# Kernel tuning notes

Measured on AMD Instinct MI355X. Metric: run time of the kernel, lower is better.

Reference implementation:

```python
import jax, jax.numpy as jnp
import numpy as np

B, H, W, D, C, K, ITERS = 16, 64, 64, 64, 16, 5, 4
EPS_LN = 1e-5

def _ln(x, g, b):
    m = x.mean(-1, keepdims=True)
    v = jnp.mean((x - m) ** 2, axis=-1, keepdims=True)
    return (x - m) / jnp.sqrt(v + EPS_LN) * g + b

def _build_grid(h, w):
    # (h, w, 2) with x in [-1,1] over width, y in [-1,1] over height
    y, x = jnp.meshgrid(jnp.linspace(-1.0, 1.0, h), jnp.linspace(-1.0, 1.0, w), indexing='ij')
    return jnp.stack([x, y], axis=-1)

def _forward(feat, feat_color, mask, slot_noise, slots_mu, slots_logsigma,
             w_grid, b_grid, w_k, w_v, ln_kv_g, ln_kv_b, w_mlp, b_mlp,
             ln_q_g, ln_q_b, w_q, w_ih, w_hh, b_ih, b_hh,
             ln_feat_g, ln_feat_b, ln_color_g, ln_color_b,
             ln_res_g, ln_res_b, w_res, b_res):
    b, h, w, d = feat.shape
    n = h * w
    k_slots = mask.shape[0]
    scale = d ** (-0.5)

    grid = _build_grid(h, w)  # (H, W, 2)

    # fg position: weighted mean of grid under mask -> (K, 2), broadcast to (B, K, 2)
    gm = grid.transpose(2, 0, 1)[None] * mask            # (K, 2, H, W)
    fg_pos = gm.sum((2, 3)) / (mask.sum((2, 3)) + 1e-5)  # (K, 2)
    fg_pos = jnp.broadcast_to(fg_pos[None], (b, k_slots, 2))

    feat_n = _ln(feat.reshape(b, n, d), ln_feat_g, ln_feat_b)                    # (B, N, D)
    featc_n = _ln(feat_color.reshape(b, n, feat_color.shape[-1]), ln_color_g, ln_color_b)

    slot = slots_mu + jnp.exp(slots_logsigma) * slot_noise  # (B, K, D)

    # k/v with relative positional grid embedding (fg_pos is constant across iters,
    # so k/v are iteration-invariant and computed once -- same math as the original loop)
    rel = grid[None, None] - fg_pos[:, :, None, None, :]        # (B, K, H, W, 2)
    rel4 = jnp.concatenate([rel, -rel], -1).reshape(b, k_slots, n, 4)
    grid_embed = rel4 @ w_grid.T + b_grid                       # (B, K, N, D)
    k = _ln(feat_n @ w_k.T[None] [0][None][0][None][0] if False else (feat_n @ w_k.T)[:, None] + grid_embed, ln_kv_g, ln_kv_b) @ w_mlp.T + b_mlp
    v = _ln((feat_n @ w_v.T)[:, None] + grid_embed, ln_kv_g, ln_kv_b) @ w_mlp.T + b_mlp

    attn = None
    for it in range(ITERS):
        prev = slot
        q = _ln(slot, ln_q_g, ln_q_b) @ w_q.T                         # (B, K, D)
        logits = jnp.einsum('bkd,bknd->bkn', q, k) * scale
        attn = jax.nn.softmax(logits, axis=-1)                        # (B, K, N)
        upd = jnp.einsum('bkn,bknd->bkd', attn, v)                    # (B, K, D)
        if it != ITERS - 1:
            # torch GRUCell
            x = upd.reshape(-1, d)
            hp = slot.reshape(-1, d)
            gi = x @ w_ih.T + b_ih
            gh = hp @ w_hh.T + b_hh
            i_r, i_z, i_n = jnp.split(gi, 3, axis=-1)
            h_r, h_z, h_n = jnp.split(gh, 3, axis=-1)
            r = jax.nn.sigmoid(i_r + h_r)
            z = jax.nn.sigmoid(i_z + h_z)
            nn_ = jnp.tanh(i_n + r * h_n)
            slot = ((1.0 - z) * nn_ + z * hp).reshape(b, k_slots, d)
            slot = _ln(slot, ln_res_g, ln_res_b) @ w_res.T + b_res + prev
        else:
            slot_color = jnp.einsum('bkn,bnc->bkc', attn, featc_n)
            slot = jnp.concatenate([slot, slot_color], axis=-1)       # (B, K, D+C)

    amin = attn.min(axis=2, keepdims=True)
    amax = attn.max(axis=2, keepdims=True)
    attn = (attn - amin) / (amax - amin + 1e-5)
    return slot, fg_pos, attn

def setup_inputs() -> dict:
    key = jax.random.key(0)
    ks = jax.random.split(key, 16)
    def rn(i, shape, s=0.02):
        return jax.random.normal(ks[i], shape, jnp.float32) * s
    return {
        'feat': jax.random.normal(ks[0], (B, H, W, D), jnp.float32),
        'feat_color': jax.random.normal(ks[1], (B, H, W, C), jnp.float32),
        'mask': jax.random.uniform(ks[2], (K, 1, H, W), jnp.float32),
        'slot_noise': jax.random.normal(ks[3], (B, K, D), jnp.float32),
        'slots_mu': rn(4, (1, 1, D), 1.0),
        'slots_logsigma': rn(5, (1, 1, D), 0.01),
        'w_grid': rn(6, (D, 4)), 'b_grid': jnp.zeros((D,), jnp.float32),
        'w_k': rn(7, (D, D)), 'w_v': rn(8, (D, D)),
        'ln_kv_g': jnp.ones((D,), jnp.float32), 'ln_kv_b': jnp.zeros((D,), jnp.float32),
        'w_mlp': rn(9, (D, D)), 'b_mlp': jnp.zeros((D,), jnp.float32),
        'ln_q_g': jnp.ones((D,), jnp.float32), 'ln_q_b': jnp.zeros((D,), jnp.float32),
        'w_q': rn(10, (D, D)),
        'w_ih': rn(11, (3 * D, D)), 'w_hh': rn(12, (3 * D, D)),
        'b_ih': jnp.zeros((3 * D,), jnp.float32), 'b_hh': jnp.zeros((3 * D,), jnp.float32),
        'ln_feat_g': jnp.ones((D,), jnp.float32), 'ln_feat_b': jnp.zeros((D,), jnp.float32),
        'ln_color_g': jnp.ones((C,), jnp.float32), 'ln_color_b': jnp.zeros((C,), jnp.float32),
        'ln_res_g': jnp.ones((D,), jnp.float32), 'ln_res_b': jnp.zeros((D,), jnp.float32),
        'w_res': rn(13, (D, D)), 'b_res': jnp.zeros((D,), jnp.float32),
    }

def reference(feat, feat_color, mask, slot_noise, slots_mu, slots_logsigma,
              w_grid, b_grid, w_k, w_v, ln_kv_g, ln_kv_b, w_mlp, b_mlp,
              ln_q_g, ln_q_b, w_q, w_ih, w_hh, b_ih, b_hh,
              ln_feat_g, ln_feat_b, ln_color_g, ln_color_b,
              ln_res_g, ln_res_b, w_res, b_res):
    return _forward(feat, feat_color, mask, slot_noise, slots_mu, slots_logsigma,
                    w_grid, b_grid, w_k, w_v, ln_kv_g, ln_kv_b, w_mlp, b_mlp,
                    ln_q_g, ln_q_b, w_q, w_ih, w_hh, b_ih, b_hh,
                    ln_feat_g, ln_feat_b, ln_color_g, ln_color_b,
                    ln_res_g, ln_res_b, w_res, b_res)
```

## Files before the change

### kernel.cpp

```cpp
#include <hip/hip_runtime.h>
#include <stdint.h>

#define B_ 16
#define H_ 64
#define W_ 64
#define D_ 64
#define C_ 16
#define K_ 5
#define N_ 4096
#define NC_ 32
#define CS_ 128
#define EPS 1e-5f

typedef __attribute__((ext_vector_type(8))) short bf16x8;
typedef __attribute__((ext_vector_type(4))) float f32x4;

__device__ __forceinline__ float wsum64(float v){
  #pragma unroll
  for(int o=1;o<64;o<<=1) v += __shfl_xor(v,o,64);
  return v;
}
__device__ __forceinline__ float wmax64(float v){
  #pragma unroll
  for(int o=1;o<64;o<<=1) v = fmaxf(v, __shfl_xor(v,o,64));
  return v;
}
__device__ __forceinline__ float wmin64(float v){
  #pragma unroll
  for(int o=1;o<64;o<<=1) v = fminf(v, __shfl_xor(v,o,64));
  return v;
}
__device__ __forceinline__ uint16_t f2bf(float f){
  uint32_t u = __float_as_uint(f);
  u += 0x7fffu + ((u>>16)&1u);
  return (uint16_t)(u>>16);
}

__global__ __launch_bounds__(256) void k_pre(
    const float* __restrict__ mask, const float* __restrict__ noise,
    const float* __restrict__ mu, const float* __restrict__ lsg,
    const float* __restrict__ wm, const float* __restrict__ bm, const float* __restrict__ lnkb,
    const float* __restrict__ wk, const float* __restrict__ wv, const float* __restrict__ lnfb,
    const float* __restrict__ wq, const float* __restrict__ lnqg, const float* __restrict__ lnqb,
    const float* __restrict__ wres, const float* __restrict__ bres,
    const float* __restrict__ lnrg, const float* __restrict__ lnrb,
    const float* __restrict__ wih, const float* __restrict__ whh,
    const float* __restrict__ wg, const float* __restrict__ bg,
    float* __restrict__ ws_fg, float* __restrict__ out_fg,
    float* __restrict__ bm2, float* __restrict__ fkb, float* __restrict__ fvb,
    float* __restrict__ qb, float* __restrict__ br2,
    float* __restrict__ wgx, float* __restrict__ wgy, float* __restrict__ gscal,
    float* __restrict__ wqpT, float* __restrict__ wrpT,
    float* __restrict__ wvT, float* __restrict__ wmT,
    float* __restrict__ gw, float* __restrict__ slot, float* __restrict__ out_slot){
  int bid=blockIdx.x, tid=threadIdx.x;
  if(bid<5){
    int k=bid;
    float sm=0.f, sx=0.f, sy=0.f;
    for(int p=tid; p<H_*W_; p+=256){
      int i=p>>6, j=p&63;
      float m = mask[k*H_*W_ + p];
      float x = -1.f + (2.f/63.f)*j;
      float y = -1.f + (2.f/63.f)*i;
      sm+=m; sx+=m*x; sy+=m*y;
    }
    __shared__ float r0[4], r1[4], r2[4];
    int wid=tid>>6, lane=tid&63;
    sm=wsum64(sm); sx=wsum64(sx); sy=wsum64(sy);
    if(lane==0){ r0[wid]=sm; r1[wid]=sx; r2[wid]=sy; }
    __syncthreads();
    if(tid==0){
      float tm=r0[0]+r0[1]+r0[2]+r0[3];
      float tx=r1[0]+r1[1]+r1[2]+r1[3];
      float ty=r2[0]+r2[1]+r2[2]+r2[3];
      float px = tx/(tm+1e-5f), py = ty/(tm+1e-5f);
      ws_fg[k*2+0]=px; ws_fg[k*2+1]=py;
      for(int b=0;b<B_;b++){ out_fg[(b*K_+k)*2+0]=px; out_fg[(b*K_+k)*2+1]=py; }
// ... 18 lines not shown
      t=wsum64(wy);    if(l==0) gscal[1]=t*(1.f/64.f);
      t=wsum64(bl);    if(l==0) gscal[2]=t*(1.f/64.f);
      t=wsum64(wx*wx); if(l==0) gscal[3]=t*(1.f/64.f);
      t=wsum64(wy*wy); if(l==0) gscal[4]=t*(1.f/64.f);
      t=wsum64(wx*wy); if(l==0) gscal[5]=t*(2.f/64.f);
      t=wsum64(wx*bl); if(l==0) gscal[6]=t*(2.f/64.f);
      t=wsum64(wy*bl); if(l==0) gscal[7]=t*(2.f/64.f);
      t=wsum64(bl*bl); if(l==0) gscal[8]=t*(1.f/64.f);
    } else {
      for(int j=l;j<B_*K_*16;j+=64){ int bk2=j>>4, cc2=j&15; out_slot[bk2*80+64+cc2]=0.f; }
    }
  } else if(bid<71){
    int i=(bid-7)*256+tid;
    int a=i>>12, r=i&4095, d=r>>6, o=r&63;
    if(a==0)      wqpT[r]=0.125f*lnqg[d]*wq[o*64+d];
    else if(a==1) wrpT[r]=lnrg[d]*wres[o*64+d];
    else if(a==2) wvT[r]=wv[o*64+d];
    else          wmT[r]=wm[o*64+d];
  } else if(bid<167){
    int i=(bid-71)*256+tid;
    int g6=i>>12, r=i&4095, d=r>>6, o=r&63;
    float v = (g6<3)? wih[(g6*64+o)*64+d] : whh[((g6-3)*64+o)*64+d];
    gw[g6*4096 + d*64 + o] = v;
  } else {
    int i=(bid-167)*256+tid;
    if(i<B_*K_*D_){ int d=i&63; slot[i]=mu[d]+expf(lsg[d])*noise[i]; }
  }
}

__global__ __launch_bounds__(256) void k_featln(const float* __restrict__ feat,
    const float* __restrict__ wk, const float* __restrict__ wv, const float* __restrict__ gf,
    const float* __restrict__ fkb, const float* __restrict__ fvb,
    const float* __restrict__ wgx, const float* __restrict__ wgy, const float* __restrict__ bg,
    const float* __restrict__ fc, const float* __restrict__ gc, const float* __restrict__ bc,
    uint16_t* __restrict__ Aout, float4* __restrict__ kstat, float4* __restrict__ vstat,
    float* __restrict__ fcn){
  int tid=threadIdx.x, wid=tid>>6, lane=tid&63;
  int q=lane>>4, c=lane&15;
  size_t row = (size_t)blockIdx.x*64 + wid*16 + c;
  const float* xp = feat + row*64;
  float x[16];
  *(float4*)&x[0]  = *(const float4*)(xp + q*8);
  *(float4*)&x[4]  = *(const float4*)(xp + q*8 + 4);
  *(float4*)&x[8]  = *(const float4*)(xp + 32 + q*8);
  *(float4*)&x[12] = *(const float4*)(xp + 36 + q*8);
  float s=0.f;
  #pragma unroll
  for(int i=0;i<16;i++) s+=x[i];
  s += __shfl_xor(s,16,64); s += __shfl_xor(s,32,64);
// ... 55 lines not shown
    if(lane<16){
      size_t row2 = (size_t)blockIdx.x*64 + wid*16 + lane;
      float4 st = { ss*(1.f/64.f), s2*(1.f/64.f)+db*(1.f/32.f), dx*(1.f/32.f), dy*(1.f/32.f) };
      (mat? vstat : kstat)[row2] = st;
    }
  }
  int r16=tid>>4, cc=tid&15;
  #pragma unroll
  for(int i=0;i<4;i++){
    size_t row2 = (size_t)blockIdx.x*64 + i*16 + r16;
    float xv = fc[row2*16+cc];
    float sc=xv;
    #pragma unroll
    for(int o=1;o<16;o<<=1) sc += __shfl_xor(sc,o,16);
    float m2 = sc*(1.f/16.f);
    float df = xv-m2;
    float v2 = df*df;
    #pragma unroll
    for(int o=1;o<16;o<<=1) v2 += __shfl_xor(v2,o,16);
    fcn[row2*16+cc] = df*rsqrtf(v2*(1.f/16.f)+EPS)*gc[cc] + bc[cc];
  }
}

template<bool GRU>
__global__ __launch_bounds__(256) void k_slotq(
    const float* __restrict__ slot_prev, float* __restrict__ slot_cur,
    const float* __restrict__ part, const float* __restrict__ pscal,
    const float* __restrict__ red_in,
    const float* __restrict__ gw,
    const float* __restrict__ bih, const float* __restrict__ bhh,
    const float* __restrict__ wrpT, const float* __restrict__ br2,
    const float* __restrict__ wqpT, const float* __restrict__ qb,
    const float* __restrict__ wm, const float* __restrict__ wk,
    const float* __restrict__ lnfg, const float* __restrict__ lnkg,
    const float* __restrict__ fkb, const float* __restrict__ bm2, const float* __restrict__ fvb,
    const float* __restrict__ wvT, const float* __restrict__ wmT,
    const float* __restrict__ wgx, const float* __restrict__ wgy, const float* __restrict__ bg,
    const float* __restrict__ gscal,
    float* __restrict__ qs_out, float* __restrict__ cst_out){
  __shared__ float vv[64], vh[64];
  __shared__ float red6[4][64][6];
  __shared__ float lamb[NC_];
  int bk=blockIdx.x;
  int tid=threadIdx.x, wid=tid>>6, lane=tid&63;
  int o=lane, qq=wid;
  float mwgx=gscal[0], mwgy=gscal[1], mbg=gscal[2];

  #define MV(Wptr) { float p_=0.f; \
      _Pragma("unroll") \
      for(int dd=0;dd<16;dd++) p_ = fmaf(vv[qq*16+dd], (Wptr)[(qq*16+dd)*64+o], p_); \
      red6[qq][o][0]=p_; } __syncthreads();
  #define SUM0 (red6[0][lane][0]+red6[1][lane][0]+red6[2][lane][0]+red6[3][lane][0])

  float cur=0.f, qv=0.f, qp=0.f, hp=0.f;
  if(GRU){
    float As=0.f, Ax=0.f, Ay=0.f, Am=0.f;
    if(wid==0){
      float m_l = (lane<NC_)? red_in[((size_t)bk*NC_+lane)*4]   : -1e30f;
      float s_l = (lane<NC_)? red_in[((size_t)bk*NC_+lane)*4+1] : 0.f;
      float M = wmax64(m_l);
      float eu = (lane<NC_)? __expf(m_l-M) : 0.f;
      float S = wsum64(s_l*eu);
      float lam = eu/S;
      if(lane<NC_) lamb[lane]=lam;
      float p0 = (lane<NC_)? pscal[((size_t)bk*NC_+lane)*4+0] : 0.f;
      float p1 = (lane<NC_)? pscal[((size_t)bk*NC_+lane)*4+1] : 0.f;
      float p2 = (lane<NC_)? pscal[((size_t)bk*NC_+lane)*4+2] : 0.f;
      float p3 = (lane<NC_)? pscal[((size_t)bk*NC_+lane)*4+3] : 0.f;
      As = wsum64(lam*p0); Ax = wsum64(lam*p1);
      Ay = wsum64(lam*p2); Am = wsum64(lam*p3);
    }
    __syncthreads();
    {
      float p_=0.f;
      #pragma unroll
      for(int j=0;j<8;j++){
        int cc = qq*8+j;
        p_ = fmaf(lamb[cc], part[((size_t)bk*NC_+cc)*64+o], p_);
      }
      red6[qq][o][0]=p_;
    }
    __syncthreads();
    if(wid==0){
      float sA = SUM0;
      vv[lane] = lnfg[lane]*sA;
    }
    __syncthreads();
    MV(wvT);
    if(wid==0){
      float fvs = SUM0 + fvb[lane]*As;
      float zs = fvs + Ax*wgx[lane] + Ay*wgy[lane] + As*bg[lane] - Am;
      vv[lane] = lnkg[lane]*zs;
    }
    __syncthreads();
    MV(wmT);
    if(wid==0){
      float x_ = SUM0 + bm2[lane];
      hp = slot_prev[bk*64+lane];
      vv[lane]=x_; vh[lane]=hp;
    }
    __syncthreads();
    {
      float p0=0.f,p1=0.f,p2=0.f,p3=0.f,p4=0.f,p5=0.f;
      #pragma unroll
      for(int dd=0;dd<16;dd++){
        int d = qq*16+dd;
        float xd=vv[d], hd=vh[d];
        p0 = fmaf(xd, gw[d*64+o], p0);
        p1 = fmaf(xd, gw[4096+d*64+o], p1);
        p2 = fmaf(xd, gw[8192+d*64+o], p2);
        p3 = fmaf(hd, gw[12288+d*64+o], p3);
        p4 = fmaf(hd, gw[16384+d*64+o], p4);
        p5 = fmaf(hd, gw[20480+d*64+o], p5);
      }
      red6[qq][o][0]=p0; red6[qq][o][1]=p1; red6[qq][o][2]=p2;
      red6[qq][o][3]=p3; red6[qq][o][4]=p4; red6[qq][o][5]=p5;
    }
    __syncthreads();
    if(wid==0){
      float gir=bih[lane], giz=bih[64+lane], gin=bih[128+lane];
      float ghr=bhh[lane], ghz=bhh[64+lane], ghn=bhh[128+lane];
      #pragma unroll
      for(int w=0;w<4;w++){
        gir+=red6[w][lane][0]; giz+=red6[w][lane][1]; gin+=red6[w][lane][2];
        ghr+=red6[w][lane][3]; ghz+=red6[w][lane][4]; ghn+=red6[w][lane][5];
      }
      float r=1.f/(1.f+__expf(-(gir+ghr)));
      float z=1.f/(1.f+__expf(-(giz+ghz)));
      float nn=tanhf(gin+r*ghn);
      float sp=(1.f-z)*nn+z*hp;
      float m=wsum64(sp)*(1.f/64.f); float df=sp-m;
      float var=wsum64(df*df)*(1.f/64.f);
      vv[lane]=df*rsqrtf(var+EPS);
    }
    __syncthreads();
    MV(wrpT);
    if(wid==0){
      cur = SUM0 + br2[lane] + hp;
      slot_cur[bk*64+lane]=cur;
    }
  } else {
    if(wid==0) cur = slot_prev[bk*64+lane];
  }
  __syncthreads();
  if(wid==0){
    float m=wsum64(cur)*(1.f/64.f); float df=cur-m;
    float var=wsum64(df*df)*(1.f/64.f);
    vv[lane]=df*rsqrtf(var+EPS);
  }
  __syncthreads();
  MV(wqpT);
  if(wid==0){ qv = SUM0 + qb[lane]; vv[lane]=qv; }
  __syncthreads();
  MV(wm);
  if(wid==0){ qp = SUM0*lnkg[lane]; vv[lane]=qp; }
  __syncthreads();
  MV(wk);
  if(wid==0){
    qs_out[bk*64+lane] = SUM0*lnfg[lane];
    float s1 = wsum64(qp);
    float c1 = wsum64(qp*wgx[lane]);
    float c2 = wsum64(qp*wgy[lane]);
    float c3 = wsum64(qp*(bg[lane]+fkb[lane]));
    float c4c = wsum64(qv*bm2[lane]);
    if(lane==0){
      float* cp = cst_out + bk*8;
      cp[0]=c1-s1*mwgx; cp[1]=c2-s1*mwgy; cp[2]=c3-s1*mbg; cp[3]=s1; cp[4]=c4c;
    }
  }
  #undef MV
  #undef SUM0
}

template<bool FINAL>
__global__ __launch_bounds__(256) void k_attn(const uint16_t* __restrict__ Aw,
    const float4* __restrict__ kstat, const float4* __restrict__ vstat,
    const float* __restrict__ qsg, const float* __restrict__ cstg,
    const float* __restrict__ gscal, const float* __restrict__ ws_fg,
    float* __restrict__ lgt, float* __restrict__ red_out,
    float* __restrict__ part_o, float* __restrict__ pscal_o){
  __shared__ uint32_t As_[CS_*32];
  __shared__ float dps[5][CS_+4];
  __shared__ float pw[4][5][64];
  __shared__ float rm[2][5], rn[2][5];
  __shared__ float rsc[2][5][5];
  __shared__ float cstl[5][5];
  __shared__ float fgl[5][2];
  int chunk=blockIdx.x, b=blockIdx.y;
  int tid=threadIdx.x, wid=tid>>6, lane=tid&63;
  int c=lane&15, q=lane>>4;
  float mwgx=gscal[0], mwgy=gscal[1], mbg=gscal[2];
  float g1=gscal[3], g2=gscal[4], g3=gscal[5], g4=gscal[6], g5=gscal[7], g6=gscal[8];

  const uint4* Ag = (const uint4*)(Aw + ((size_t)b*N_ + chunk*CS_)*64);
  #pragma unroll
  for(int jj=0;jj<4;jj++){
    int f = jj*256 + tid;
    *(uint4*)(As_ + f*4) = Ag[f];
  }
  if(tid<25) cstl[tid/5][tid%5] = cstg[(b*K_ + tid/5)*8 + (tid%5)];
  if(tid>=32 && tid<42){ int i2=tid-32; fgl[i2>>1][i2&1] = ws_fg[i2]; }
  bool act = tid < CS_;
  int nrow = chunk*CS_ + (tid & (CS_-1));
  float4 st, sv;
  float gx=0.f, gy=0.f;
  if(act){
    st = kstat[(size_t)b*N_ + nrow];
    if(!FINAL) sv = vstat[(size_t)b*N_ + nrow];
    gx = -1.f + (2.f/63.f)*(nrow&63);
    gy = -1.f + (2.f/63.f)*(nrow>>6);
  }
  __syncthreads();

  {
    bf16x8 QF0={0,0,0,0,0,0,0,0}, QF1={0,0,0,0,0,0,0,0};
    if(c<5){
      const float* qpp = qsg + (b*K_+c)*64;
      #pragma unroll
      for(int j=0;j<8;j++){
        QF0[j] = (short)f2bf(qpp[q*8+j]);
        QF1[j] = (short)f2bf(qpp[32+q*8+j]);
      }
    }
    const uint16_t* Abase = Aw + ((size_t)b*N_ + chunk*CS_)*64;
    #pragma unroll
    for(int it=0;it<2;it++){
      int tile = wid*32 + it*16;
      const uint16_t* rp = Abase + (size_t)(tile+c)*64;
      bf16x8 BF0 = *(const bf16x8*)(rp + q*8);
      bf16x8 BF1 = *(const bf16x8*)(rp + 32 + q*8);
      f32x4 acc = {0.f,0.f,0.f,0.f};
      acc = __builtin_amdgcn_mfma_f32_16x16x32_bf16(QF0, BF0, acc, 0,0,0);
      acc = __builtin_amdgcn_mfma_f32_16x16x32_bf16(QF1, BF1, acc, 0,0,0);
      #pragma unroll
      for(int r=0;r<4;r++){
        int s = q*4+r;
        if(s<5) dps[s][tile+c]=acc[r];
      }
    }
  }
// ... 15 lines not shown
      if(lane==0) rm[wid][k]=wmx;
      if(FINAL){ float mn=wmin64(l); if(lane==0) rn[wid][k]=mn; }
    }
  }
  __syncthreads();
  if(act){
    #pragma unroll
    for(int k=0;k<5;k++){
      float m_c = fmaxf(rm[0][k], rm[1][k]);
      float e = __expf(l5[k]-m_c);
      float scq = wsum64(e);
      if(!FINAL){
        float rx = gx - fgl[k][0], ry = gy - fgl[k][1];
        float quad = g1*rx*rx + g2*ry*ry + g3*rx*ry + g4*rx + g5*ry + g6;
        float muV = sv.x + rx*mwgx + ry*mwgy + mbg;
        float varV = sv.y + rx*sv.z + ry*sv.w + quad - muV*muV;
        float rsv_ = rsqrtf(varV+EPS);
        float w_ = e*rsv_;
        w5[k]=w_;
        float As2=wsum64(w_), Ax2=wsum64(w_*rx), Ay2=wsum64(w_*ry), Am2=wsum64(w_*muV);
        if(lane==0){ rsc[wid][k][0]=scq; rsc[wid][k][1]=As2; rsc[wid][k][2]=Ax2;
                     rsc[wid][k][3]=Ay2; rsc[wid][k][4]=Am2; }
      } else {
        lgt[(size_t)(b*K_+k)*N_ + nrow] = l5[k];
        if(lane==0) rsc[wid][k][0]=scq;
      }
    }
  }
  __syncthreads();
  if(tid<5){
    int k=tid;
    size_t idx = ((size_t)(b*K_+k)*NC_+chunk)*4;
    red_out[idx+0]=fmaxf(rm[0][k],rm[1][k]);
    red_out[idx+1]=rsc[0][k][0]+rsc[1][k][0];
    if(FINAL) red_out[idx+2]=fminf(rn[0][k],rn[1][k]);
    if(!FINAL){
      pscal_o[idx+0]=rsc[0][k][1]+rsc[1][k][1];
      pscal_o[idx+1]=rsc[0][k][2]+rsc[1][k][2];
      pscal_o[idx+2]=rsc[0][k][3]+rsc[1][k][3];
      pscal_o[idx+3]=rsc[0][k][4]+rsc[1][k][4];
    }
  }
  if(act && !FINAL){
    #pragma unroll
    for(int k=0;k<5;k++) dps[k][tid]=w5[k];
  }

  if(!FINAL){
    __syncthreads();
    const uint16_t* Au = (const uint16_t*)As_;
    float a[5]={0.f,0.f,0.f,0.f,0.f};
    for(int r32=0;r32<32;r32++){
      int row = wid*32 + r32;
      float av = __uint_as_float(((uint32_t)Au[row*64+lane])<<16);
      #pragma unroll
      for(int k=0;k<5;k++) a[k]=fmaf(dps[k][row], av, a[k]);
    }
    #pragma unroll
    for(int k=0;k<5;k++) pw[wid][k][lane]=a[k];
    __syncthreads();
    if(tid<64){
      #pragma unroll
      for(int k=0;k<5;k++){
        float s2 = pw[0][k][tid]+pw[1][k][tid]+pw[2][k][tid]+pw[3][k][tid];
        part_o[((size_t)(b*K_+k)*NC_+chunk)*64 + tid] = s2;
      }
    }
  }
}

__global__ __launch_bounds__(256) void k_fin(const float* __restrict__ lgt,
    const float* __restrict__ red, const float* __restrict__ featc,
    const float* __restrict__ sl1, float* __restrict__ out_slot,
    float* __restrict__ out_attn){
  __shared__ float psp[CS_];
  __shared__ float pcz[4][16];
  int chunk=blockIdx.x, bk=blockIdx.y, b=bk/K_;
  int tid=threadIdx.x, wid=tid>>6, lane=tid&63, sub=lane>>4, c4=lane&15;
  const float* rp = red + (size_t)bk*NC_*4;
  float M=-1e30f;
  #pragma unroll
  for(int i=0;i<NC_;i++) M = fmaxf(M, rp[i*4]);
  float S=0.f;
  #pragma unroll
  for(int i=0;i<NC_;i++) S += rp[i*4+1]*__expf(rp[i*4]-M);
  float invS = 1.f/S;
  float LMIN=1e30f;
  #pragma unroll
// ... 57 lines not shown
  const float* wres = (const float*)d_in[27];
  const float* bres = (const float*)d_in[28];

  float* out = (float*)d_out;
  float* out_slot = out;
  float* out_fg   = out + 6400;
  float* out_attn = out + 6560;

  float* wsf     = (float*)d_ws;
  float* ws_fg   = wsf;
  float* ws_bm2  = wsf + 16;
  float* ws_fkb  = ws_bm2 + 64;
  float* ws_fvb  = ws_fkb + 64;
  float* ws_qb   = ws_fvb + 64;
  float* ws_br2  = ws_qb + 64;
  float* ws_wgx  = ws_br2 + 64;
  float* ws_wgy  = ws_wgx + 64;
  float* ws_gs   = ws_wgy + 64;
  float* ws_wqpT = ws_gs + 16;
  float* ws_wrpT = ws_wqpT + 4096;
  float* ws_wvT  = ws_wrpT + 4096;
  float* ws_wmT  = ws_wvT + 4096;
  float* ws_gw   = ws_wmT + 4096;
  float* ws_fc   = ws_gw + 24576;
  float* ws_sl0  = ws_fc + (size_t)B_*N_*C_;
  float* ws_sl1  = ws_sl0 + B_*K_*D_;
  float* ws_qs   = ws_sl1 + B_*K_*D_;
  float* ws_cst  = ws_qs + B_*K_*D_;
  float* ws_lgt  = ws_cst + 640;
  float* ws_red0 = ws_lgt + (size_t)B_*K_*N_;
  float* ws_red1 = ws_red0 + B_*K_*NC_*4;
  float* ws_prt0 = ws_red1 + B_*K_*NC_*4;
  float* ws_prt1 = ws_prt0 + (size_t)B_*K_*NC_*64;
  float* ws_psc0 = ws_prt1 + (size_t)B_*K_*NC_*64;
  float* ws_psc1 = ws_psc0 + B_*K_*NC_*4;
  float4* ws_kst = (float4*)(ws_psc1 + B_*K_*NC_*4);
  float4* ws_vst = ws_kst + (size_t)B_*N_;
  uint16_t* ws_A = (uint16_t*)(ws_vst + (size_t)B_*N_);

  k_pre<<<187,256,0,stream>>>(mask,noise,mu,lsg, wm,bm,lnkb, wk,wv,lnfb,
                              wq,lnqg,lnqb, wres,bres,lnrg,lnrb, wih,whh, wg,bg,
                              ws_fg,out_fg, ws_bm2,ws_fkb,ws_fvb,ws_qb,ws_br2,
                              ws_wgx,ws_wgy,ws_gs,
                              ws_wqpT,ws_wrpT,ws_wvT,ws_wmT, ws_gw, ws_sl0, out_slot);
  k_featln<<<(B_*N_)/64,256,0,stream>>>(feat,wk,wv,lnfg,ws_fkb,ws_fvb,
                                        ws_wgx,ws_wgy,bg,
                                        featc,lncg,lncb,
                                        ws_A,ws_kst,ws_vst,ws_fc);

  dim3 agrid(NC_,B_);
  #define SQ_ARGS(SPREV,SCUR,PIN,SCIN,RIN) SPREV,SCUR,PIN,SCIN,RIN,ws_gw, \
      bih,bhh,ws_wrpT,ws_br2,ws_wqpT,ws_qb, wm,wk,lnfg,lnkg, \
      ws_fkb,ws_bm2,ws_fvb, ws_wvT,ws_wmT, ws_wgx,ws_wgy,bg, ws_gs, ws_qs,ws_cst
  #define AT_ARGS(ROUT,POUT,SCOUT) ws_A,ws_kst,ws_vst,ws_qs,ws_cst,ws_gs,ws_fg, \
      ws_lgt,ROUT,POUT,SCOUT

  k_slotq<false><<<B_*K_,256,0,stream>>>(SQ_ARGS(ws_sl0,ws_sl0,ws_prt1,ws_psc1,ws_red1));
  k_attn<false><<<agrid,256,0,stream>>>(AT_ARGS(ws_red0,ws_prt0,ws_psc0));
  k_slotq<true><<<B_*K_,256,0,stream>>>(SQ_ARGS(ws_sl0,ws_sl1,ws_prt0,ws_psc0,ws_red0));
  k_attn<false><<<agrid,256,0,stream>>>(AT_ARGS(ws_red1,ws_prt1,ws_psc1));
  k_slotq<true><<<B_*K_,256,0,stream>>>(SQ_ARGS(ws_sl1,ws_sl0,ws_prt1,ws_psc1,ws_red1));
  k_attn<false><<<agrid,256,0,stream>>>(AT_ARGS(ws_red0,ws_prt0,ws_psc0));
  k_slotq<true><<<B_*K_,256,0,stream>>>(SQ_ARGS(ws_sl0,ws_sl1,ws_prt0,ws_psc0,ws_red0));
  k_attn<true><<<agrid,256,0,stream>>>(AT_ARGS(ws_red1,ws_prt1,ws_psc1));
  k_fin<<<dim3(NC_,B_*K_),256,0,stream>>>(ws_lgt,ws_red1,ws_fc,ws_sl1,out_slot,out_attn);
}
```

Measured before the change: 222.6 us.

## Fuse slot update and query projection into attention kernel with precomposed weights

```diff
diff --git a/kernel.cpp b/kernel.cpp
--- a/kernel.cpp
+++ b/kernel.cpp
@@ -46,13 +46,20 @@
     const float* __restrict__ lnrg, const float* __restrict__ lnrb,
     const float* __restrict__ wih, const float* __restrict__ whh,
     const float* __restrict__ wg, const float* __restrict__ bg,
+    const float* __restrict__ lnfg, const float* __restrict__ lnkg,
     float* __restrict__ ws_fg, float* __restrict__ out_fg,
     float* __restrict__ bm2, float* __restrict__ fkb, float* __restrict__ fvb,
     float* __restrict__ qb, float* __restrict__ br2,
     float* __restrict__ wgx, float* __restrict__ wgy, float* __restrict__ gscal,
     float* __restrict__ wqpT, float* __restrict__ wrpT,
     float* __restrict__ wvT, float* __restrict__ wmT,
-    float* __restrict__ gw, float* __restrict__ slot, float* __restrict__ out_slot){
+    float* __restrict__ gw, float* __restrict__ slot, float* __restrict__ out_slot,
+    float* __restrict__ WQp, float* __restrict__ WCp, float* __restrict__ bq2p,
+    float* __restrict__ uvp, float* __restrict__ vqp, float* __restrict__ cscp){
+  __shared__ float M0[64][65];
+  __shared__ float M1[64][65];
+  __shared__ float M2[64][65];
+  __shared__ float vtmp[4][64];
   int bid=blockIdx.x, tid=threadIdx.x;
   if(bid<5){
     int k=bid;
@@ -117,9 +124,60 @@
     int g6=i>>12, r=i&4095, d=r>>6, o=r&63;
     float v = (g6<3)? wih[(g6*64+o)*64+d] : whh[((g6-3)*64+o)*64+d];
     gw[g6*4096 + d*64 + o] = v;
-  } else {
+  } else if(bid<187){
     int i=(bid-167)*256+tid;
     if(i<B_*K_*D_){ int d=i&63; slot[i]=mu[d]+expf(lsg[d])*noise[i]; }
+  } else if(bid==187){
+    for(int i=tid;i<4096;i+=256){ int r=i>>6,c2=i&63; M0[r][c2]=wq[i]; M1[r][c2]=wm[i]; }
+    __syncthreads();
+    if(tid<64){ float s=0.f; for(int d=0;d<64;d++) s+=lnqb[d]*M0[tid][d]; vtmp[0][tid]=0.125f*s; }
+    else if(tid<128){ int c2=tid-64; float s=bm[c2]; for(int d=0;d<64;d++) s+=lnkb[d]*M1[c2][d]; vtmp[1][c2]=s; }
+    else if(tid<192){ int o=tid-128; float s=0.f; for(int d=0;d<64;d++) s+=lnfb[d]*wk[o*64+d]; vtmp[2][o]=s; }
+    __syncthreads();
+    for(int i=tid;i<4096;i+=256){ int d=i>>6,e=i&63; float s=0.f;
+      for(int c2=0;c2<64;c2++) s=fmaf(M0[c2][d], M1[c2][e], s);
+      M2[d][e]=0.125f*lnqg[d]*s; }
+    __syncthreads();
+    if(tid<64){
+      int e=tid; float s=0.f; for(int c2=0;c2<64;c2++) s=fmaf(vtmp[0][c2], M1[c2][e], s); vtmp[3][e]=s;
+    } else if(tid<128){
+      int d=tid-64; float s=0.f; for(int c2=0;c2<64;c2++) s=fmaf(M0[c2][d], vtmp[1][c2], s);
+      vqp[4*64+d]=0.125f*lnqg[d]*s;
+    }
+    __syncthreads();
+    for(int i=tid;i<4096;i+=256){ int e=i>>6,o=i&63; M0[e][o]=lnkg[e]*wk[i]; }
+    __syncthreads();
+    for(int i=tid;i<4096;i+=256){ int d=i>>6,o=i&63; float s=0.f;
+      for(int e=0;e<64;e++) s=fmaf(M2[d][e], M0[e][o], s);
+      WQp[i]=lnfg[o]*s; }
+    if(tid<64){ int o=tid; float s=0.f;
+      for(int e=0;e<64;e++) s=fmaf(vtmp[3][e], M0[e][o], s);
+      bq2p[o]=lnfg[o]*s; }
+    else if(tid<128){ int d=tid-64; float s1=0.f,sx=0.f,sy=0.f,s3=0.f;
+      for(int e=0;e<64;e++){ float pe=M2[d][e]*lnkg[e];
+        float gx_=wg[e*4]-wg[e*4+2], gy_=wg[e*4+1]-wg[e*4+3];
+        s1+=pe; sx+=pe*gx_; sy+=pe*gy_; s3+=pe*(bg[e]+vtmp[2][e]); }
+      vqp[0*64+d]=s1; vqp[1*64+d]=sx; vqp[2*64+d]=sy; vqp[3*64+d]=s3; }
+    else if(tid==128){ float c0=0.f,c1=0.f,c2=0.f,c3=0.f,c4=0.f;
+      for(int e=0;e<64;e++){ float qe=vtmp[3][e]*lnkg[e];
+        float gx_=wg[e*4]-wg[e*4+2], gy_=wg[e*4+1]-wg[e*4+3];
+        c0+=qe; c1+=qe*gx_; c2+=qe*gy_; c3+=qe*(bg[e]+vtmp[2][e]);
+        c4+=vtmp[0][e]*vtmp[1][e]; }
+      cscp[0]=c0; cscp[1]=c1; cscp[2]=c2; cscp[3]=c3; cscp[4]=c4; }
+  } else {
+    for(int i=tid;i<4096;i+=256){ int r=i>>6,c2=i&63; M0[r][c2]=wv[i]*lnkg[r]; M1[r][c2]=wm[i]; }
+    __syncthreads();
+    if(tid<64){ float s=0.f; const float* wr=wv+tid*64;
+      for(int d=0;d<64;d++) s+=lnfb[d]*wr[d]; vtmp[0][tid]=s; }
+    __syncthreads();
+    for(int i=tid;i<4096;i+=256){ int d=i>>6,o=i&63; float s=0.f;
+      for(int e=0;e<64;e++) s=fmaf(M0[e][d], M1[o][e], s);
+      WCp[i]=lnfg[d]*s; }
+    if(tid<64){ int o=tid; float s1=0.f,s2=0.f,s3=0.f,s4=0.f;
+      for(int e=0;e<64;e++){ float we=lnkg[e]*M1[o][e];
+        float gx_=wg[e*4]-wg[e*4+2], gy_=wg[e*4+1]-wg[e*4+3];
+        s1+=we*(vtmp[0][e]+bg[e]); s2+=we*gx_; s3+=we*gy_; s4+=we; }
+      uvp[0*64+o]=s1; uvp[1*64+o]=s2; uvp[2*64+o]=s3; uvp[3*64+o]=s4; }
   }
 }
 
@@ -221,184 +279,64 @@
   }
 }
 
-template<bool GRU>
-__global__ __launch_bounds__(256) void k_slotq(
+#define MV5(W) { \
+  float p0=0.f,p1=0.f,p2=0.f,p3=0.f,p4=0.f; \
+  _Pragma("unroll") \
+  for(int d4=0;d4<4;d4++){ \
+    int d0_=wid*16+d4*4; \
+    float4 q0_=*(const float4*)&sq[0][d0_]; \
+    float4 q1_=*(const float4*)&sq[1][d0_]; \
+    float4 q2_=*(const float4*)&sq[2][d0_]; \
+    float4 q3_=*(const float4*)&sq[3][d0_]; \
+    float4 q4_=*(const float4*)&sq[4][d0_]; \
+    float w0_=(W)[(d0_+0)*64+lane]; \
+    float w1_=(W)[(d0_+1)*64+lane]; \
+    float w2_=(W)[(d0_+2)*64+lane]; \
+    float w3_=(W)[(d0_+3)*64+lane]; \
+    p0=fmaf(q0_.x,w0_,p0); p0=fmaf(q0_.y,w1_,p0); p0=fmaf(q0_.z,w2_,p0); p0=fmaf(q0_.w,w3_,p0); \
+    p1=fmaf(q1_.x,w0_,p1); p1=fmaf(q1_.y,w1_,p1); p1=fmaf(q1_.z,w2_,p1); p1=fmaf(q1_.w,w3_,p1); \
+    p2=fmaf(q2_.x,w0_,p2); p2=fmaf(q2_.y,w1_,p2); p2=fmaf(q2_.z,w2_,p2); p2=fmaf(q2_.w,w3_,p2); \
+    p3=fmaf(q3_.x,w0_,p3); p3=fmaf(q3_.y,w1_,p3); p3=fmaf(q3_.z,w2_,p3); p3=fmaf(q3_.w,w3_,p3); \
+    p4=fmaf(q4_.x,w0_,p4); p4=fmaf(q4_.y,w1_,p4); p4=fmaf(q4_.z,w2_,p4); p4=fmaf(q4_.w,w3_,p4); \
+  } \
+  redp[wid][lane][0]=p0; redp[wid][lane][1]=p1; redp[wid][lane][2]=p2; \
+  redp[wid][lane][3]=p3; redp[wid][lane][4]=p4; \
+  __syncthreads(); }
+
+template<bool GRU, bool FINAL>
+__global__ __launch_bounds__(256,2) void k_attn(const uint16_t* __restrict__ Aw,
+    const float4* __restrict__ kstat, const float4* __restrict__ vstat,
+    const float* __restrict__ gscal, const float* __restrict__ ws_fg,
     const float* __restrict__ slot_prev, float* __restrict__ slot_cur,
-    const float* __restrict__ part, const float* __restrict__ pscal,
+    const float* __restrict__ part_in, const float* __restrict__ pscal_in,
     const float* __restrict__ red_in,
-    const float* __restrict__ gw,
-    const float* __restrict__ bih, const float* __restrict__ bhh,
-    const float* __restrict__ wrpT, const float* __restrict__ br2,
-    const float* __restrict__ wqpT, const float* __restrict__ qb,
-    const float* __restrict__ wm, const float* __restrict__ wk,
-    const float* __restrict__ lnfg, const float* __restrict__ lnkg,
-    const float* __restrict__ fkb, const float* __restrict__ bm2, const float* __restrict__ fvb,
-    const float* __restrict__ wvT, const float* __restrict__ wmT,
-    const float* __restrict__ wgx, const float* __restrict__ wgy, const float* __restrict__ bg,
-    const float* __restrict__ gscal,
-    float* __restrict__ qs_out, float* __restrict__ cst_out){
-  __shared__ float vv[64], vh[64];
-  __shared__ float red6[4][64][6];
-  __shared__ float lamb[NC_];
-  int bk=blockIdx.x;
-  int tid=threadIdx.x, wid=tid>>6, lane=tid&63;
-  int o=lane, qq=wid;
-  float mwgx=gscal[0], mwgy=gscal[1], mbg=gscal[2];
-
-  #define MV(Wptr) { float p_=0.f; \
-      _Pragma("unroll") \
-      for(int dd=0;dd<16;dd++) p_ = fmaf(vv[qq*16+dd], (Wptr)[(qq*16+dd)*64+o], p_); \
-      red6[qq][o][0]=p_; } __syncthreads();
-  #define SUM0 (red6[0][lane][0]+red6[1][lane][0]+red6[2][lane][0]+red6[3][lane][0])
-
-  float cur=0.f, qv=0.f, qp=0.f, hp=0.f;
-  if(GRU){
-    float As=0.f, Ax=0.f, Ay=0.f, Am=0.f;
-    if(wid==0){
-      float m_l = (lane<NC_)? red_in[((size_t)bk*NC_+lane)*4]   : -1e30f;
-      float s_l = (lane<NC_)? red_in[((size_t)bk*NC_+lane)*4+1] : 0.f;
-      float M = wmax64(m_l);
-      float eu = (lane<NC_)? __expf(m_l-M) : 0.f;
-      float S = wsum64(s_l*eu);
-      float lam = eu/S;
-      if(lane<NC_) lamb[lane]=lam;
-      float p0 = (lane<NC_)? pscal[((size_t)bk*NC_+lane)*4+0] : 0.f;
-      float p1 = (lane<NC_)? pscal[((size_t)bk*NC_+lane)*4+1] : 0.f;
-      float p2 = (lane<NC_)? pscal[((size_t)bk*NC_+lane)*4+2] : 0.f;
-      float p3 = (lane<NC_)? pscal[((size_t)bk*NC_+lane)*4+3] : 0.f;
-      As = wsum64(lam*p0); Ax = wsum64(lam*p1);
-      Ay = wsum64(lam*p2); Am = wsum64(lam*p3);
-    }
-    __syncthreads();
-    {
-      float p_=0.f;
-      #pragma unroll
-      for(int j=0;j<8;j++){
-        int cc = qq*8+j;
-        p_ = fmaf(lamb[cc], part[((size_t)bk*NC_+cc)*64+o], p_);
-      }
-      red6[qq][o][0]=p_;
-    }
-    __syncthreads();
-    if(wid==0){
-      float sA = SUM0;
-      vv[lane] = lnfg[lane]*sA;
-    }
-    __syncthreads();
-    MV(wvT);
-    if(wid==0){
-      float fvs = SUM0 + fvb[lane]*As;
-      float zs = fvs + Ax*wgx[lane] + Ay*wgy[lane] + As*bg[lane] - Am;
-      vv[lane] = lnkg[lane]*zs;
-    }
-    __syncthreads();
-    MV(wmT);
-    if(wid==0){
-      float x_ = SUM0 + bm2[lane];
-      hp = slot_prev[bk*64+lane];
-      vv[lane]=x_; vh[lane]=hp;
-    }
-    __syncthreads();
-    {
-      float p0=0.f,p1=0.f,p2=0.f,p3=0.f,p4=0.f,p5=0.f;
-      #pragma unroll
-      for(int dd=0;dd<16;dd++){
-        int d = qq*16+dd;
-        float xd=vv[d], hd=vh[d];
-        p0 = fmaf(xd, gw[d*64+o], p0);
-        p1 = fmaf(xd, gw[4096+d*64+o], p1);
-        p2 = fmaf(xd, gw[8192+d*64+o], p2);
-        p3 = fmaf(hd, gw[12288+d*64+o], p3);
-        p4 = fmaf(hd, gw[16384+d*64+o], p4);
-        p5 = fmaf(hd, gw[20480+d*64+o], p5);
-      }
-      red6[qq][o][0]=p0; red6[qq][o][1]=p1; red6[qq][o][2]=p2;
-      red6[qq][o][3]=p3; red6[qq][o][4]=p4; red6[qq][o][5]=p5;
-    }
-    __syncthreads();
-    if(wid==0){
-      float gir=bih[lane], giz=bih[64+lane], gin=bih[128+lane];
-      float ghr=bhh[lane], ghz=bhh[64+lane], ghn=bhh[128+lane];
-      #pragma unroll
-      for(int w=0;w<4;w++){
-        gir+=red6[w][lane][0]; giz+=red6[w][lane][1]; gin+=red6[w][lane][2];
-        ghr+=red6[w][lane][3]; ghz+=red6[w][lane][4]; ghn+=red6[w][lane][5];
-      }
-      float r=1.f/(1.f+__expf(-(gir+ghr)));
-      float z=1.f/(1.f+__expf(-(giz+ghz)));
-      float nn=tanhf(gin+r*ghn);
-      float sp=(1.f-z)*nn+z*hp;
-      float m=wsum64(sp)*(1.f/64.f); float df=sp-m;
-      float var=wsum64(df*df)*(1.f/64.f);
-      vv[lane]=df*rsqrtf(var+EPS);
-    }
-    __syncthreads();
-    MV(wrpT);
-    if(wid==0){
-      cur = SUM0 + br2[lane] + hp;
-      slot_cur[bk*64+lane]=cur;
-    }
-  } else {
-    if(wid==0) cur = slot_prev[bk*64+lane];
-  }
-  __syncthreads();
-  if(wid==0){
-    float m=wsum64(cur)*(1.f/64.f); float df=cur-m;
-    float var=wsum64(df*df)*(1.f/64.f);
-    vv[lane]=df*rsqrtf(var+EPS);
-  }
-  __syncthreads();
-  MV(wqpT);
-  if(wid==0){ qv = SUM0 + qb[lane]; vv[lane]=qv; }
-  __syncthreads();
-  MV(wm);
-  if(wid==0){ qp = SUM0*lnkg[lane]; vv[lane]=qp; }
-  __syncthreads();
-  MV(wk);
-  if(wid==0){
-    qs_out[bk*64+lane] = SUM0*lnfg[lane];
-    float s1 = wsum64(qp);
-    float c1 = wsum64(qp*wgx[lane]);
-    float c2 = wsum64(qp*wgy[lane]);
-    float c3 = wsum64(qp*(bg[lane]+fkb[lane]));
-    float c4c = wsum64(qv*bm2[lane]);
-    if(lane==0){
-      float* cp = cst_out + bk*8;
-      cp[0]=c1-s1*mwgx; cp[1]=c2-s1*mwgy; cp[2]=c3-s1*mbg; cp[3]=s1; cp[4]=c4c;
-    }
-  }
-  #undef MV
-  #undef SUM0
-}
-
-template<bool FINAL>
-__global__ __launch_bounds__(256) void k_attn(const uint16_t* __restrict__ Aw,
-    const float4* __restrict__ kstat, const float4* __restrict__ vstat,
-    const float* __restrict__ qsg, const float* __restrict__ cstg,
-    const float* __restrict__ gscal, const float* __restrict__ ws_fg,
+    const float* __restrict__ gw, const float* __restrict__ bih, const float* __restrict__ bhh,
+    const float* __restrict__ wrpT, const float* __restrict__ br2, const float* __restrict__ bm2,
+    const float* __restrict__ WQ, const float* __restrict__ bq2,
+    const float* __restrict__ WC, const float* __restrict__ uvec,
+    const float* __restrict__ vq, const float* __restrict__ csc,
     float* __restrict__ lgt, float* __restrict__ red_out,
     float* __restrict__ part_o, float* __restrict__ pscal_o){
   __shared__ uint32_t As_[CS_*32];
-  __shared__ float dps[5][CS_+4];
+  __shared__ __align__(16) float dps[5][CS_+4];
   __shared__ float pw[4][5][64];
   __shared__ float rm[2][5], rn[2][5];
   __shared__ float rsc[2][5][5];
   __shared__ float cstl[5][5];
   __shared__ float fgl[5][2];
+  __shared__ __align__(16) float sq[5][64];
+  __shared__ float xg[5][64];
+  __shared__ float hg[5][64];
+  __shared__ float redp[4][64][5];
+  __shared__ float lamS[5][NC_];
+  __shared__ float scal4[5][4];
   int chunk=blockIdx.x, b=blockIdx.y;
   int tid=threadIdx.x, wid=tid>>6, lane=tid&63;
   int c=lane&15, q=lane>>4;
+  int bk0=b*K_;
   float mwgx=gscal[0], mwgy=gscal[1], mbg=gscal[2];
   float g1=gscal[3], g2=gscal[4], g3=gscal[5], g4=gscal[6], g5=gscal[7], g6=gscal[8];
-
-  const uint4* Ag = (const uint4*)(Aw + ((size_t)b*N_ + chunk*CS_)*64);
-  #pragma unroll
-  for(int jj=0;jj<4;jj++){
-    int f = jj*256 + tid;
-    *(uint4*)(As_ + f*4) = Ag[f];
-  }
-  if(tid<25) cstl[tid/5][tid%5] = cstg[(b*K_ + tid/5)*8 + (tid%5)];
-  if(tid>=32 && tid<42){ int i2=tid-32; fgl[i2>>1][i2&1] = ws_fg[i2]; }
+  if(tid<10) fgl[tid>>1][tid&1]=ws_fg[tid];
   bool act = tid < CS_;
   int nrow = chunk*CS_ + (tid & (CS_-1));
   float4 st, sv;
@@ -409,12 +347,162 @@
     gx = -1.f + (2.f/63.f)*(nrow&63);
     gy = -1.f + (2.f/63.f)*(nrow>>6);
   }
+
+  if(GRU){
+    for(int s=wid; s<5; s+=4){
+      size_t base=(size_t)(bk0+s)*NC_;
+      float m_l=(lane<NC_)? red_in[(base+lane)*4]   : -1e30f;
+      float s_l=(lane<NC_)? red_in[(base+lane)*4+1] : 0.f;
+      float M=wmax64(m_l);
+      float eu=(lane<NC_)? __expf(m_l-M) : 0.f;
+      float S=wsum64(s_l*eu);
+      float lam=eu/S;
+      if(lane<NC_) lamS[s][lane]=lam;
+      float p0=(lane<NC_)? pscal_in[(base+lane)*4+0]:0.f;
+      float p1=(lane<NC_)? pscal_in[(base+lane)*4+1]:0.f;
+      float p2=(lane<NC_)? pscal_in[(base+lane)*4+2]:0.f;
+      float p3=(lane<NC_)? pscal_in[(base+lane)*4+3]:0.f;
+      float As=wsum64(lam*p0), Ax=wsum64(lam*p1), Ay=wsum64(lam*p2), Am=wsum64(lam*p3);
+      if(lane==0){ scal4[s][0]=As; scal4[s][1]=Ax; scal4[s][2]=Ay; scal4[s][3]=Am; }
+    }
+    __syncthreads();
+    #pragma unroll
+    for(int s=0;s<5;s++){
+      float p_=0.f;
+      #pragma unroll
+      for(int j=0;j<8;j++){
+        int cc=wid*8+j;
+        p_=fmaf(lamS[s][cc], part_in[((size_t)(bk0+s)*NC_+cc)*64+lane], p_);
+      }
+      redp[wid][lane][s]=p_;
+    }
+    __syncthreads();
+    for(int s=wid; s<5; s+=4)
+      sq[s][lane]=redp[0][lane][s]+redp[1][lane][s]+redp[2][lane][s]+redp[3][lane][s];
+    __syncthreads();
+    MV5(WC);
+    for(int s=wid; s<5; s+=4){
+      float As=scal4[s][0],Ax=scal4[s][1],Ay=scal4[s][2],Am=scal4[s][3];
+      float x_=redp[0][lane][s]+redp[1][lane][s]+redp[2][lane][s]+redp[3][lane][s]
+              + As*uvec[lane] + Ax*uvec[64+lane] + Ay*uvec[128+lane] - Am*uvec[192+lane]
+              + bm2[lane];
+      xg[s][lane]=x_;
+      hg[s][lane]=slot_prev[(bk0+s)*64+lane];
+    }
+    __syncthreads();
+    {
+      float pr[5]={0,0,0,0,0}, pz[5]={0,0,0,0,0}, pi[5]={0,0,0,0,0}, ph[5]={0,0,0,0,0};
+      #pragma unroll
+      for(int dd=0;dd<16;dd++){
+        int d=wid*16+dd;
+        float g0_=gw[d*64+lane],       g1_=gw[4096+d*64+lane],  g2_=gw[8192+d*64+lane];
+        float g3_=gw[12288+d*64+lane], g4_=gw[16384+d*64+lane], g5_=gw[20480+d*64+lane];
+        #pragma unroll
+        for(int s=0;s<5;s++){
+          float xd=xg[s][d], hd=hg[s][d];
+          pr[s]=fmaf(xd,g0_,pr[s]); pr[s]=fmaf(hd,g3_,pr[s]);
+          pz[s]=fmaf(xd,g1_,pz[s]); pz[s]=fmaf(hd,g4_,pz[s]);
+          pi[s]=fmaf(xd,g2_,pi[s]);
+          ph[s]=fmaf(hd,g5_,ph[s]);
+        }
+      }
+      float* redG=(float*)As_;
+      #pragma unroll
+      for(int s=0;s<4;s++){
+        redG[(s*4+0)*256+tid]=pr[s];
+        redG[(s*4+1)*256+tid]=pz[s];
+        redG[(s*4+2)*256+tid]=pi[s];
+        redG[(s*4+3)*256+tid]=ph[s];
+      }
+      redp[wid][lane][0]=pr[4]; redp[wid][lane][1]=pz[4];
+      redp[wid][lane][2]=pi[4]; redp[wid][lane][3]=ph[4];
+    }
+    __syncthreads();
+    for(int s=wid; s<5; s+=4){
+      const float* redG=(const float*)As_;
+      float pr_,pz_,pi_,ph_;
+      if(s<4){
+        int b0=(s*4+0)*256, b1=(s*4+1)*256, b2=(s*4+2)*256, b3=(s*4+3)*256;
+        pr_=redG[b0+lane]+redG[b0+64+lane]+redG[b0+128+lane]+redG[b0+192+lane];
+        pz_=redG[b1+lane]+redG[b1+64+lane]+redG[b1+128+lane]+redG[b1+192+lane];
+        pi_=redG[b2+lane]+redG[b2+64+lane]+redG[b2+128+lane]+redG[b2+192+lane];
+        ph_=redG[b3+lane]+redG[b3+64+lane]+redG[b3+128+lane]+redG[b3+192+lane];
+      } else {
+        pr_=redp[0][lane][0]+redp[1][lane][0]+redp[2][lane][0]+redp[3][lane][0];
+        pz_=redp[0][lane][1]+redp[1][lane][1]+redp[2][lane][1]+redp[3][lane][1];
+        pi_=redp[0][lane][2]+redp[1][lane][2]+redp[2][lane][2]+redp[3][lane][2];
+        ph_=redp[0][lane][3]+redp[1][lane][3]+redp[2][lane][3]+redp[3][lane][3];
+      }
+      float r=1.f/(1.f+__expf(-(pr_+bih[lane]+bhh[lane])));
+      float z=1.f/(1.f+__expf(-(pz_+bih[64+lane]+bhh[64+lane])));
+      float nn=tanhf(pi_+bih[128+lane] + r*(ph_+bhh[128+lane]));
+      float hp=hg[s][lane];
+      float sp=(1.f-z)*nn+z*hp;
+      float m=wsum64(sp)*(1.f/64.f);
+      float df=sp-m;
+      float var=wsum64(df*df)*(1.f/64.f);
+      sq[s][lane]=df*rsqrtf(var+EPS);
+    }
+    __syncthreads();
+    MV5(wrpT);
+    for(int s=wid; s<5; s+=4){
+      float cur=redp[0][lane][s]+redp[1][lane][s]+redp[2][lane][s]+redp[3][lane][s]
+               + br2[lane] + hg[s][lane];
+      if(chunk==0) slot_cur[(bk0+s)*64+lane]=cur;
+      float m=wsum64(cur)*(1.f/64.f);
+      float df=cur-m;
+      float var=wsum64(df*df)*(1.f/64.f);
+      float LNc=df*rsqrtf(var+EPS);
+      sq[s][lane]=LNc;
+      float s1=wsum64(LNc*vq[lane])     + csc[0];
+      float c1=wsum64(LNc*vq[64+lane])  + csc[1];
+      float c2=wsum64(LNc*vq[128+lane]) + csc[2];
+      float c3=wsum64(LNc*vq[192+lane]) + csc[3];
+      float c4=wsum64(LNc*vq[256+lane]) + csc[4];
+      if(lane==0){
+        cstl[s][0]=c1-s1*mwgx; cstl[s][1]=c2-s1*mwgy; cstl[s][2]=c3-s1*mbg;
+        cstl[s][3]=s1; cstl[s][4]=c4;
+      }
+    }
+    __syncthreads();
+  } else {
+    for(int s=wid; s<5; s+=4){
+      float cur=slot_prev[(bk0+s)*64+lane];
+      float m=wsum64(cur)*(1.f/64.f);
+      float df=cur-m;
+      float var=wsum64(df*df)*(1.f/64.f);
+      float LNc=df*rsqrtf(var+EPS);
+      sq[s][lane]=LNc;
+      float s1=wsum64(LNc*vq[lane])     + csc[0];
+      float c1=wsum64(LNc*vq[64+lane])  + csc[1];
+      float c2=wsum64(LNc*vq[128+lane]) + csc[2];
+      float c3=wsum64(LNc*vq[192+lane]) + csc[3];
+      float c4=wsum64(LNc*vq[256+lane]) + csc[4];
+      if(lane==0){
+        cstl[s][0]=c1-s1*mwgx; cstl[s][1]=c2-s1*mwgy; cstl[s][2]=c3-s1*mbg;
+        cstl[s][3]=s1; cstl[s][4]=c4;
+      }
+    }
+    __syncthreads();
+  }
+  MV5(WQ);
+  for(int s=wid; s<5; s+=4)
+    xg[s][lane]=redp[0][lane][s]+redp[1][lane][s]+redp[2][lane][s]+redp[3][lane][s] + bq2[lane];
   __syncthreads();
+
+  if(!FINAL){
+    const uint4* Ag = (const uint4*)(Aw + ((size_t)b*N_ + chunk*CS_)*64);
+    #pragma unroll
+    for(int jj=0;jj<4;jj++){
+      int f = jj*256 + tid;
+      *(uint4*)(As_ + f*4) = Ag[f];
+    }
+  }
 
   {
     bf16x8 QF0={0,0,0,0,0,0,0,0}, QF1={0,0,0,0,0,0,0,0};
     if(c<5){
-      const float* qpp = qsg + (b*K_+c)*64;
+      const float* qpp = &xg[c][0];
       #pragma unroll
       for(int j=0;j<8;j++){
         QF0[j] = (short)f2bf(qpp[q*8+j]);
@@ -476,7 +564,7 @@
         if(lane==0){ rsc[wid][k][0]=scq; rsc[wid][k][1]=As2; rsc[wid][k][2]=Ax2;
                      rsc[wid][k][3]=Ay2; rsc[wid][k][4]=Am2; }
       } else {
-        lgt[(size_t)(b*K_+k)*N_ + nrow] = l5[k];
+        lgt[(size_t)(bk0+k)*N_ + nrow] = l5[k];
         if(lane==0) rsc[wid][k][0]=scq;
       }
     }
@@ -484,7 +572,7 @@
   __syncthreads();
   if(tid<5){
     int k=tid;
-    size_t idx = ((size_t)(b*K_+k)*NC_+chunk)*4;
+    size_t idx = ((size_t)(bk0+k)*NC_+chunk)*4;
     red_out[idx+0]=fmaxf(rm[0][k],rm[1][k]);
     red_out[idx+1]=rsc[0][k][0]+rsc[1][k][0];
     if(FINAL) red_out[idx+2]=fminf(rn[0][k],rn[1][k]);
@@ -503,21 +591,33 @@
   if(!FINAL){
     __syncthreads();
     const uint16_t* Au = (const uint16_t*)As_;
-    float a[5]={0.f,0.f,0.f,0.f,0.f};
-    for(int r32=0;r32<32;r32++){
-      int row = wid*32 + r32;
-      float av = __uint_as_float(((uint32_t)Au[row*64+lane])<<16);
-      #pragma unroll
-      for(int k=0;k<5;k++) a[k]=fmaf(dps[k][row], av, a[k]);
-    }
-    #pragma unroll
-    for(int k=0;k<5;k++) pw[wid][k][lane]=a[k];
+    float a0=0.f,a1=0.f,a2=0.f,a3=0.f,a4=0.f;
+    #pragma unroll
+    for(int rb=0;rb<8;rb++){
+      int row0 = wid*32 + rb*4;
+      float4 d0 = *(const float4*)&dps[0][row0];
+      float4 d1 = *(const float4*)&dps[1][row0];
+      float4 d2 = *(const float4*)&dps[2][row0];
+      float4 d3 = *(const float4*)&dps[3][row0];
+      float4 d4 = *(const float4*)&dps[4][row0];
+      float av0 = __uint_as_float(((uint32_t)Au[(row0+0)*64+lane])<<16);
+      float av1 = __uint_as_float(((uint32_t)Au[(row0+1)*64+lane])<<16);
+      float av2 = __uint_as_float(((uint32_t)Au[(row0+2)*64+lane])<<16);
+      float av3 = __uint_as_float(((uint32_t)Au[(row0+3)*64+lane])<<16);
+      a0=fmaf(d0.x,av0,a0); a0=fmaf(d0.y,av1,a0); a0=fmaf(d0.z,av2,a0); a0=fmaf(d0.w,av3,a0);
+      a1=fmaf(d1.x,av0,a1); a1=fmaf(d1.y,av1,a1); a1=fmaf(d1.z,av2,a1); a1=fmaf(d1.w,av3,a1);
+      a2=fmaf(d2.x,av0,a2); a2=fmaf(d2.y,av1,a2); a2=fmaf(d2.z,av2,a2); a2=fmaf(d2.w,av3,a2);
+      a3=fmaf(d3.x,av0,a3); a3=fmaf(d3.y,av1,a3); a3=fmaf(d3.z,av2,a3); a3=fmaf(d3.w,av3,a3);
+      a4=fmaf(d4.x,av0,a4); a4=fmaf(d4.y,av1,a4); a4=fmaf(d4.z,av2,a4); a4=fmaf(d4.w,av3,a4);
+    }
+    pw[wid][0][lane]=a0; pw[wid][1][lane]=a1; pw[wid][2][lane]=a2;
+    pw[wid][3][lane]=a3; pw[wid][4][lane]=a4;
     __syncthreads();
     if(tid<64){
       #pragma unroll
       for(int k=0;k<5;k++){
         float s2 = pw[0][k][tid]+pw[1][k][tid]+pw[2][k][tid]+pw[3][k][tid];
-        part_o[((size_t)(b*K_+k)*NC_+chunk)*64 + tid] = s2;
+        part_o[((size_t)(bk0+k)*NC_+chunk)*64 + tid] = s2;
       }
     }
   }
@@ -621,12 +721,16 @@
   float* ws_wvT  = ws_wrpT + 4096;
   float* ws_wmT  = ws_wvT + 4096;
   float* ws_gw   = ws_wmT + 4096;
-  float* ws_fc   = ws_gw + 24576;
+  float* ws_WQ   = ws_gw + 24576;
+  float* ws_WC   = ws_WQ + 4096;
+  float* ws_bq2  = ws_WC + 4096;
+  float* ws_u    = ws_bq2 + 64;
+  float* ws_vq   = ws_u + 256;
+  float* ws_csc  = ws_vq + 320;
+  float* ws_fc   = ws_csc + 16;
   float* ws_sl0  = ws_fc + (size_t)B_*N_*C_;
   float* ws_sl1  = ws_sl0 + B_*K_*D_;
-  float* ws_qs   = ws_sl1 + B_*K_*D_;
-  float* ws_cst  = ws_qs + B_*K_*D_;
-  float* ws_lgt  = ws_cst + 640;
+  float* ws_lgt  = ws_sl1 + B_*K_*D_;
   float* ws_red0 = ws_lgt + (size_t)B_*K_*N_;
   float* ws_red1 = ws_red0 + B_*K_*NC_*4;
   float* ws_prt0 = ws_red1 + B_*K_*NC_*4;
@@ -637,30 +741,29 @@
   float4* ws_vst = ws_kst + (size_t)B_*N_;
   uint16_t* ws_A = (uint16_t*)(ws_vst + (size_t)B_*N_);
 
-  k_pre<<<187,256,0,stream>>>(mask,noise,mu,lsg, wm,bm,lnkb, wk,wv,lnfb,
+  k_pre<<<189,256,0,stream>>>(mask,noise,mu,lsg, wm,bm,lnkb, wk,wv,lnfb,
                               wq,lnqg,lnqb, wres,bres,lnrg,lnrb, wih,whh, wg,bg,
+                              lnfg,lnkg,
                               ws_fg,out_fg, ws_bm2,ws_fkb,ws_fvb,ws_qb,ws_br2,
                               ws_wgx,ws_wgy,ws_gs,
-                              ws_wqpT,ws_wrpT,ws_wvT,ws_wmT, ws_gw, ws_sl0, out_slot);
+                              ws_wqpT,ws_wrpT,ws_wvT,ws_wmT, ws_gw, ws_sl0, out_slot,
+                              ws_WQ, ws_WC, ws_bq2, ws_u, ws_vq, ws_csc);
   k_featln<<<(B_*N_)/64,256,0,stream>>>(feat,wk,wv,lnfg,ws_fkb,ws_fvb,
                                         ws_wgx,ws_wgy,bg,
                                         featc,lncg,lncb,
                                         ws_A,ws_kst,ws_vst,ws_fc);
 
   dim3 agrid(NC_,B_);
-  #define SQ_ARGS(SPREV,SCUR,PIN,SCIN,RIN) SPREV,SCUR,PIN,SCIN,RIN,ws_gw, \
-      bih,bhh,ws_wrpT,ws_br2,ws_wqpT,ws_qb, wm,wk,lnfg,lnkg, \
-      ws_fkb,ws_bm2,ws_fvb, ws_wvT,ws_wmT, ws_wgx,ws_wgy,bg, ws_gs, ws_qs,ws_cst
-  #define AT_ARGS(ROUT,POUT,SCOUT) ws_A,ws_kst,ws_vst,ws_qs,ws_cst,ws_gs,ws_fg, \
-      ws_lgt,ROUT,POUT,SCOUT
-
-  k_slotq<false><<<B_*K_,256,0,stream>>>(SQ_ARGS(ws_sl0,ws_sl0,ws_prt1,ws_psc1,ws_red1));
-  k_attn<false><<<agrid,256,0,stream>>>(AT_ARGS(ws_red0,ws_prt0,ws_psc0));
-  k_slotq<true><<<B_*K_,256,0,stream>>>(SQ_ARGS(ws_sl0,ws_sl1,ws_prt0,ws_psc0,ws_red0));
-  k_attn<false><<<agrid,256,0,stream>>>(AT_ARGS(ws_red1,ws_prt1,ws_psc1));
-  k_slotq<true><<<B_*K_,256,0,stream>>>(SQ_ARGS(ws_sl1,ws_sl0,ws_prt1,ws_psc1,ws_red1));
-  k_attn<false><<<agrid,256,0,stream>>>(AT_ARGS(ws_red0,ws_prt0,ws_psc0));
-  k_slotq<true><<<B_*K_,256,0,stream>>>(SQ_ARGS(ws_sl0,ws_sl1,ws_prt0,ws_psc0,ws_red0));
-  k_attn<true><<<agrid,256,0,stream>>>(AT_ARGS(ws_red1,ws_prt1,ws_psc1));
+  #define ATT_COMMON ws_A,ws_kst,ws_vst,ws_gs,ws_fg
+  #define ATT_W ws_gw,bih,bhh,ws_wrpT,ws_br2,ws_bm2,ws_WQ,ws_bq2,ws_WC,ws_u,ws_vq,ws_csc
+
+  k_attn<false,false><<<agrid,256,0,stream>>>(ATT_COMMON, ws_sl0, ws_sl1,
+      ws_prt1, ws_psc1, ws_red1, ATT_W, ws_lgt, ws_red0, ws_prt0, ws_psc0);
+  k_attn<true,false><<<agrid,256,0,stream>>>(ATT_COMMON, ws_sl0, ws_sl1,
+      ws_prt0, ws_psc0, ws_red0, ATT_W, ws_lgt, ws_red1, ws_prt1, ws_psc1);
+  k_attn<true,false><<<agrid,256,0,stream>>>(ATT_COMMON, ws_sl1, ws_sl0,
+      ws_prt1, ws_psc1, ws_red1, ATT_W, ws_lgt, ws_red0, ws_prt0, ws_psc0);
+  k_attn<true,true><<<agrid,256,0,stream>>>(ATT_COMMON, ws_sl0, ws_sl1,
+      ws_prt0, ws_psc0, ws_red0, ATT_W, ws_lgt, ws_red1, ws_prt1, ws_psc1);
   k_fin<<<dim3(NC_,B_*K_),256,0,stream>>>(ws_lgt,ws_red1,ws_fc,ws_sl1,out_slot,out_attn);
 }
```

Result: slower. 258.5 us (+16.1%).
